# Performance work log

Hardware: AMD Instinct MI355X
Metric: run time of the kernel (lower is better)

Reference implementation:

```python
import jax, jax.numpy as jnp
import numpy as np

N_HEAD = 4
IN_FEAT = 512
N_FEAT = 512
D_K = N_FEAT // N_HEAD
KERNEL = 11
SANM_SHIFT = 0
LEFT_PAD = (KERNEL - 1) // 2 + SANM_SHIFT
RIGHT_PAD = KERNEL - 1 - LEFT_PAD
B, T = 16, 1024
NEG = -1e9  # stand-in for -inf (grad-safe)


def setup_inputs() -> dict:
    key = jax.random.key(0)
    ks = jax.random.split(key, 6)
    x = jax.random.normal(ks[0], (B, T, IN_FEAT), dtype=jnp.float32)
    # padding mask: first 3/4 of frames valid, tail padded (as in batched ASR)
    valid = (jnp.arange(T) < (3 * T) // 4).astype(jnp.float32)
    mask = jnp.broadcast_to(valid[None, None, :], (B, 1, T))
    s = 1.0 / np.sqrt(IN_FEAT)
    w_qkv = jax.random.uniform(ks[1], (IN_FEAT, 3 * N_FEAT), jnp.float32, -s, s)
    b_qkv = jnp.zeros((3 * N_FEAT,), jnp.float32)
    so = 1.0 / np.sqrt(N_FEAT)
    w_out = jax.random.uniform(ks[2], (N_FEAT, N_FEAT), jnp.float32, -so, so)
    b_out = jnp.zeros((N_FEAT,), jnp.float32)
    # depthwise Conv1d weight: (channels, k)
    w_fsmn = jax.random.uniform(ks[3], (N_FEAT, KERNEL), jnp.float32, -1.0 / np.sqrt(KERNEL), 1.0 / np.sqrt(KERNEL))
    return {"x": x, "mask": mask, "w_qkv": w_qkv, "b_qkv": b_qkv,
            "w_out": w_out, "b_out": b_out, "w_fsmn": w_fsmn}


def _fsmn(v, mask_bt1, w_fsmn):
    # v: (B,T,D); mask_bt1: (B,T,1)
    inp = v * mask_bt1
    xc = jnp.transpose(inp, (0, 2, 1))                      # (B,D,T)
    xc = jnp.pad(xc, ((0, 0), (0, 0), (LEFT_PAD, RIGHT_PAD)))
    y = jax.lax.conv_general_dilated(
        xc, w_fsmn[:, None, :], window_strides=(1,), padding='VALID',
        feature_group_count=N_FEAT, dimension_numbers=('NCH', 'OIH', 'NCH'))
    y = jnp.transpose(y, (0, 2, 1)) + inp                   # residual
    return y * mask_bt1                                     # re-zero padded frames


def _forward(x, mask, w_qkv, b_qkv, w_out, b_out, w_fsmn):
    b, t, _ = x.shape
    qkv = x @ w_qkv + b_qkv                                 # (B,T,3D)
    q, k, v = jnp.split(qkv, 3, axis=-1)
    qh = q.reshape(b, t, N_HEAD, D_K).transpose(0, 2, 1, 3) # (B,H,T,dk)
    kh = k.reshape(b, t, N_HEAD, D_K).transpose(0, 2, 1, 3)
    vh = v.reshape(b, t, N_HEAD, D_K).transpose(0, 2, 1, 3)

    fsmn_mem = _fsmn(v, mask.reshape(b, t, 1), w_fsmn)

    scale = D_K ** (-0.5)
    scores = jnp.einsum('bhqd,bhkd->bhqk', qh * scale, kh)  # (B,H,T,T)
    m0 = (mask[:, None, :, :] == 0)                         # (B,1,1,T)
    scores = jnp.where(m0, NEG, scores)
    attn = jax.nn.softmax(scores, axis=-1)
    attn = jnp.where(m0, 0.0, attn)
    ctx = jnp.einsum('bhqk,bhkd->bhqd', attn, vh)
    ctx = ctx.transpose(0, 2, 1, 3).reshape(b, t, N_FEAT)
    att_out = ctx @ w_out + b_out
    return att_out + fsmn_mem


def reference(x, mask, w_qkv, b_qkv, w_out, b_out, w_fsmn):
    return _forward(x, mask, w_qkv, b_qkv, w_out, b_out, w_fsmn)
```

## Files before the change

kernel.cpp:

```cpp
#include <hip/hip_runtime.h>
#include <stdint.h>

#define SCALE_Q 0.08838834764831845f
#define LOG2E 1.4426950408889634f
#define NEGBIG -1e30f

typedef __attribute__((ext_vector_type(4))) float f32x4;
typedef __attribute__((ext_vector_type(16))) float f32x16;
typedef __attribute__((ext_vector_type(8))) short s16x8;
typedef __attribute__((ext_vector_type(4))) unsigned u32x4;

static __device__ __forceinline__ unsigned short f2bf(float f) {
  unsigned int u = __builtin_bit_cast(unsigned int, f);
  u += 0x7FFFu + ((u >> 16) & 1u);
  return (unsigned short)(u >> 16);
}

static __device__ __forceinline__ unsigned cvt_pk_bf16(float lo, float hi) {
  unsigned r;
  asm("v_cvt_pk_bf16_f32 %0, %1, %2" : "=v"(r) : "v"(lo), "v"(hi));
  return r;
}

static __device__ __forceinline__ float xchg_max(float x) {
  float a = x, b = x;
  asm("v_permlane32_swap_b32 %0, %1" : "+v"(a), "+v"(b));
  return fmaxf(a, b);
}
static __device__ __forceinline__ float xchg_sum(float x) {
  float a = x, b = x;
  asm("v_permlane32_swap_b32 %0, %1" : "+v"(a), "+v"(b));
  return a + b;
}

static __device__ __forceinline__ float vmax16(const f32x16& v) {
  float a = fmaxf(fmaxf(fmaxf(v[0], v[1]), fmaxf(v[2], v[3])),
                  fmaxf(fmaxf(v[4], v[5]), fmaxf(v[6], v[7])));
  float b = fmaxf(fmaxf(fmaxf(v[8], v[9]), fmaxf(v[10], v[11])),
                  fmaxf(fmaxf(v[12], v[13]), fmaxf(v[14], v[15])));
  return fmaxf(a, b);
}

__global__ void k_convert_x(const float* __restrict__ x, unsigned short* __restrict__ xb) {
  int i = (blockIdx.x * 256 + threadIdx.x) * 8;
  const float4* p = reinterpret_cast<const float4*>(x + i);
  float4 a = p[0], b = p[1];
  s16x8 o;
  o[0] = f2bf(a.x); o[1] = f2bf(a.y); o[2] = f2bf(a.z); o[3] = f2bf(a.w);
  o[4] = f2bf(b.x); o[5] = f2bf(b.y); o[6] = f2bf(b.z); o[7] = f2bf(b.w);
  *reinterpret_cast<s16x8*>(xb + i) = o;
}

__global__ void k_transpose_bf(const float* __restrict__ w, unsigned short* __restrict__ wt, int Nd) {
  int gid = blockIdx.x * 256 + threadIdx.x;
  int n = gid >> 6;
  int k0 = (gid & 63) * 8;
  if (n >= Nd) return;
  s16x8 o;
#pragma unroll
  for (int j = 0; j < 8; ++j) o[j] = f2bf(w[(size_t)(k0 + j) * Nd + n]);
  *reinterpret_cast<s16x8*>(wt + (size_t)n * 512 + k0) = o;
}

template <int MODE>
__launch_bounds__(256, 2)
__global__ void k_gemm(const unsigned short* __restrict__ A,
                       const unsigned short* __restrict__ Bt,
                       const float* __restrict__ bias,
                       const float* __restrict__ fsmn,
                       unsigned short* __restrict__ qs, unsigned short* __restrict__ kbuf,
                       float* __restrict__ vf, unsigned short* __restrict__ vt,
                       float* __restrict__ outp,
                       int tiles_m) {
  __shared__ unsigned short a_lds[128 * 64];
  __shared__ unsigned short b_lds[128 * 64];
  int bid = blockIdx.x;
  int rb = bid % tiles_m, cb = bid / tiles_m;
  int tid = threadIdx.x;
  int w = tid >> 6, lane = tid & 63;
  int g = lane >> 4, ln = lane & 15;
  int wr = w >> 1, wc = w & 1;

  f32x4 acc[4][4] = {};

  for (int kb0 = 0; kb0 < 512; kb0 += 64) {
#pragma unroll
    for (int it = 0; it < 4; ++it) {
      int chunk = it * 256 + tid;
      int r = chunk >> 3, c = chunk & 7;
      s16x8 va = *reinterpret_cast<const s16x8*>(A + (size_t)(rb * 128 + r) * 512 + kb0 + c * 8);
      s16x8 vb = *reinterpret_cast<const s16x8*>(Bt + (size_t)(cb * 128 + r) * 512 + kb0 + c * 8);
      *reinterpret_cast<s16x8*>(a_lds + r * 64 + ((c ^ (r & 7)) * 8)) = va;
      *reinterpret_cast<s16x8*>(b_lds + r * 64 + ((c ^ (r & 7)) * 8)) = vb;
    }
    __syncthreads();
#pragma unroll
    for (int kk = 0; kk < 2; ++kk) {
      s16x8 af[4], bf[4];
#pragma unroll
      for (int m = 0; m < 4; ++m) {
        int row = wr * 64 + m * 16 + ln;
        af[m] = *reinterpret_cast<const s16x8*>(a_lds + row * 64 + ((kk * 32 + g * 8) ^ ((row & 7) * 8)));
      }
#pragma unroll
      for (int n = 0; n < 4; ++n) {
        int row = wc * 64 + n * 16 + ln;
        bf[n] = *reinterpret_cast<const s16x8*>(b_lds + row * 64 + ((kk * 32 + g * 8) ^ ((row & 7) * 8)));
      }
#pragma unroll
      for (int m = 0; m < 4; ++m)
#pragma unroll
        for (int n = 0; n < 4; ++n)
          acc[m][n] = __builtin_amdgcn_mfma_f32_16x16x32_bf16(af[m], bf[n], acc[m][n], 0, 0, 0);
    }
    __syncthreads();
  }

  int c0 = cb * 128;
  int R0 = rb * 128 + wr * 64;
#pragma unroll
  for (int m = 0; m < 4; ++m) {
#pragma unroll
    for (int n = 0; n < 4; ++n) {
      int col = c0 + wc * 64 + n * 16 + ln;
      int Rbase = R0 + m * 16 + g * 4;
      if constexpr (MODE == 0) {
        float bv = bias[col];
        int which = col >> 9;
        int h = (col >> 7) & 3;
        int d = col & 127;
        int b = Rbase >> 10, t0 = Rbase & 1023;
        if (which == 2) {
          unsigned short pk[4];
#pragma unroll
          for (int r = 0; r < 4; ++r) {
            float v = acc[m][n][r] + bv;
            vf[(size_t)(Rbase + r) * 512 + (col - 1024)] = v;
            pk[r] = f2bf(v);
          }
          uint2 uv;
          uv.x = (unsigned)pk[0] | ((unsigned)pk[1] << 16);
          uv.y = (unsigned)pk[2] | ((unsigned)pk[3] << 16);
          *reinterpret_cast<uint2*>(vt + ((size_t)((b * 4 + h) * 128 + d)) * 1024 + t0) = uv;
        } else {
          unsigned short* dst = (which == 0) ? qs : kbuf;
          float sc = (which == 0) ? (SCALE_Q * LOG2E) : 1.0f;
#pragma unroll
          for (int r = 0; r < 4; ++r) {
            int t = t0 + r;
            dst[((size_t)((b * 4 + h) * 1024 + t)) * 128 + d] = f2bf((acc[m][n][r] + bv) * sc);
          }
        }
      } else {
        float bv = bias[col];
#pragma unroll
        for (int r = 0; r < 4; ++r) {
          size_t idx = (size_t)(Rbase + r) * 512 + col;
          outp[idx] = acc[m][n][r] + bv + fsmn[idx];
        }
      }
    }
  }
}

__launch_bounds__(256, 2)
__global__ void k_fsmn(const float* __restrict__ vf, const float* __restrict__ mask,
                       const float* __restrict__ wf, float* __restrict__ out) {
  __shared__ float inp[266 * 64];
  __shared__ float wl[64 * 13];
  int bid = blockIdx.x;
  int b = bid >> 5;
  int tt = (bid >> 3) & 3;
  int dt = bid & 7;
  int t0 = tt * 256, d0 = dt * 64;
  int tid = threadIdx.x;
  if (tid < 64) {
#pragma unroll
    for (int j = 0; j < 11; ++j) wl[tid * 13 + j] = wf[(d0 + tid) * 11 + j];
  }
  for (int idx = tid; idx < 266 * 64; idx += 256) {
    int r = idx >> 6, c = idx & 63;
    int t = t0 - 5 + r;
    float v = 0.f;
    if (t >= 0 && t < 1024) v = vf[((size_t)b * 1024 + t) * 512 + d0 + c] * mask[b * 1024 + t];
    inp[idx] = v;
  }
  __syncthreads();
  for (int idx = tid; idx < 256 * 64; idx += 256) {
    int tr = idx >> 6, c = idx & 63;
    int t = t0 + tr;
    float acc = inp[(tr + 5) * 64 + c];
#pragma unroll
    for (int j = 0; j < 11; ++j) acc += inp[(tr + j) * 64 + c] * wl[c * 13 + j];
    out[((size_t)b * 1024 + t) * 512 + d0 + c] = acc * mask[b * 1024 + t];
  }
}

__launch_bounds__(512, 1)
__global__ void k_attn(const unsigned short* __restrict__ qs,
                       const unsigned short* __restrict__ kbuf,
                       const unsigned short* __restrict__ vt,
                       const float* __restrict__ mask,
                       unsigned short* __restrict__ ctx) {
  __shared__ unsigned short smem[2 * 128 * 128];
  __shared__ float mask_lds[128];
  unsigned short* k_lds = smem;
  unsigned short* vt_lds = smem + 128 * 128;

  int bid = blockIdx.x;
  int qc = bid & 3;
  int bh = bid >> 2;
  int b = bh >> 2, h = bh & 3;
  int tid = threadIdx.x;
  int w = tid >> 6, l = tid & 63;
  int half = l >> 5, lq = l & 31;

  const unsigned short* kbase = kbuf + (size_t)bh * 1024 * 128;
  const unsigned short* vtbase = vt + (size_t)bh * 128 * 1024;
  const float* mbase = mask + b * 1024;

  s16x8 aq[8];
  {
    const unsigned short* qrow = qs + ((size_t)bh * 1024 + qc * 256 + w * 32 + lq) * 128 + half * 8;
#pragma unroll
    for (int c = 0; c < 8; ++c)
      aq[c] = *reinterpret_cast<const s16x8*>(qrow + c * 16);
  }

  s16x8 bone = {};
  bone[0] = (short)(half == 0 ? 0x3F80 : 0);

  f32x16 o[4] = {};
  float M = NEGBIG, L = 0.f;

  for (int kb = 0; kb < 8; ++kb) {
    float m0 = mbase[kb * 128 + l];
    float m1 = mbase[kb * 128 + 64 + l];
    if (__ballot((m0 != 0.f) || (m1 != 0.f)) == 0ull) continue;

    __syncthreads();
#pragma unroll
    for (int it = 0; it < 4; ++it) {
      int chunk = it * 512 + tid;
      int r = chunk >> 4, c = chunk & 15;
      s16x8 kv = *reinterpret_cast<const s16x8*>(kbase + (size_t)(kb * 128 + r) * 128 + c * 8);
      *reinterpret_cast<s16x8*>(k_lds + r * 128 + ((c ^ (r & 15)) * 8)) = kv;
      s16x8 vv = *reinterpret_cast<const s16x8*>(vtbase + (size_t)r * 1024 + kb * 128 + c * 8);
      *reinterpret_cast<s16x8*>(vt_lds + r * 128 + ((c ^ (r & 15)) * 8)) = vv;
    }
    if (tid < 128) mask_lds[tid] = mbase[kb * 128 + tid];
    __syncthreads();

    f32x16 s[4];
#pragma unroll
    for (int kt = 0; kt < 4; ++kt) {
      float mv = mask_lds[kt * 32 + lq];
      s16x8 ba = {};
      ba[0] = (short)((half == 0 && mv == 0.f) ? (short)0xFF7F : 0);
      f32x16 z = {};
      s[kt] = __builtin_amdgcn_mfma_f32_32x32x16_bf16(ba, bone, z, 0, 0, 0);
      int row = kt * 32 + lq, rx = row & 15;
#pragma unroll
      for (int c = 0; c < 8; ++c) {
        s16x8 kf = *reinterpret_cast<const s16x8*>(k_lds + row * 128 + (((c * 2 + half) ^ rx) * 8));
        s[kt] = __builtin_amdgcn_mfma_f32_32x32x16_bf16(kf, aq[c], s[kt], 0, 0, 0);
      }
    }

    float mx = fmaxf(fmaxf(vmax16(s[0]), vmax16(s[1])), fmaxf(vmax16(s[2]), vmax16(s[3])));
    mx = xchg_max(mx);
    float mnew = fmaxf(M, mx);
    float alpha = exp2f(M - mnew);
    M = mnew;
    float ls0 = 0.f, ls1 = 0.f, ls2 = 0.f, ls3 = 0.f;
#pragma unroll
    for (int kt = 0; kt < 4; ++kt) {
#pragma unroll
      for (int i = 0; i < 16; ++i) {
        float p = exp2f(s[kt][i] - M);
        s[kt][i] = p;
        if ((i & 3) == 0) ls0 += p; else if ((i & 3) == 1) ls1 += p;
        else if ((i & 3) == 2) ls2 += p; else ls3 += p;
      }
    }
    float ls = (ls0 + ls1) + (ls2 + ls3);
    ls = xchg_sum(ls);
    L = L * alpha + ls;
#pragma unroll
    for (int dt = 0; dt < 4; ++dt)
#pragma unroll
      for (int i = 0; i < 16; ++i) o[dt][i] *= alpha;

#pragma unroll
    for (int kt = 0; kt < 4; ++kt) {
      unsigned w0 = cvt_pk_bf16(s[kt][0], s[kt][1]);
      unsigned w1 = cvt_pk_bf16(s[kt][2], s[kt][3]);
      unsigned w2 = cvt_pk_bf16(s[kt][4], s[kt][5]);
      unsigned w3 = cvt_pk_bf16(s[kt][6], s[kt][7]);
      unsigned w4 = cvt_pk_bf16(s[kt][8], s[kt][9]);
      unsigned w5 = cvt_pk_bf16(s[kt][10], s[kt][11]);
      unsigned w6 = cvt_pk_bf16(s[kt][12], s[kt][13]);
      unsigned w7 = cvt_pk_bf16(s[kt][14], s[kt][15]);
      asm("v_permlane32_swap_b32 %0, %1" : "+v"(w0), "+v"(w2));
      asm("v_permlane32_swap_b32 %0, %1" : "+v"(w1), "+v"(w3));
      asm("v_permlane32_swap_b32 %0, %1" : "+v"(w4), "+v"(w6));
      asm("v_permlane32_swap_b32 %0, %1" : "+v"(w5), "+v"(w7));
      u32x4 f0 = {w0, w1, w2, w3};
      u32x4 f1 = {w4, w5, w6, w7};
      s16x8 p0 = __builtin_bit_cast(s16x8, f0);
      s16x8 p1 = __builtin_bit_cast(s16x8, f1);
#pragma unroll
      for (int dt = 0; dt < 4; ++dt) {
        int row = dt * 32 + lq, rx = row & 15;
        s16x8 va = *reinterpret_cast<const s16x8*>(vt_lds + row * 128 + (((kt * 4 + half) ^ rx) * 8));
        o[dt] = __builtin_amdgcn_mfma_f32_32x32x16_bf16(va, p0, o[dt], 0, 0, 0);
        s16x8 vb = *reinterpret_cast<const s16x8*>(vt_lds + row * 128 + (((kt * 4 + 2 + half) ^ rx) * 8));
        o[dt] = __builtin_amdgcn_mfma_f32_32x32x16_bf16(vb, p1, o[dt], 0, 0, 0);
      }
    }
  }

  float inv = 1.0f / L;
  __syncthreads();
  unsigned short* obuf = smem;
#pragma unroll
  for (int dt = 0; dt < 4; ++dt) {
#pragma unroll
    for (int g = 0; g < 4; ++g) {
      int d0 = dt * 32 + g * 8 + half * 4;
      unsigned lo = cvt_pk_bf16(o[dt][g * 4 + 0] * inv, o[dt][g * 4 + 1] * inv);
      unsigned hi = cvt_pk_bf16(o[dt][g * 4 + 2] * inv, o[dt][g * 4 + 3] * inv);
      int row = w * 32 + lq;
      int gr = d0 >> 2;
      uint2 uv; uv.x = lo; uv.y = hi;
      *reinterpret_cast<uint2*>(obuf + row * 128 + ((gr ^ (row & 15)) * 4)) = uv;
    }
  }
  __syncthreads();
  size_t cbase = ((size_t)b * 1024 + qc * 256) * 512 + h * 128;
#pragma unroll
  for (int it = 0; it < 16; ++it) {
    int chunk = it * 512 + tid;
    int row = chunk >> 5, gr = chunk & 31;
    uint2 v = *reinterpret_cast<uint2*>(obuf + row * 128 + ((gr ^ (row & 15)) * 4));
    *reinterpret_cast<uint2*>(ctx + cbase + (size_t)row * 512 + gr * 4) = v;
  }
}

extern "C" void kernel_launch(void* const* d_in, const int* in_sizes, int n_in,
                              void* d_out, int out_size, void* d_ws, size_t ws_size,
                              hipStream_t stream) {
  const float* x      = (const float*)d_in[0];
  const float* mask   = (const float*)d_in[1];
  const float* w_qkv  = (const float*)d_in[2];
  const float* b_qkv  = (const float*)d_in[3];
  const float* w_out  = (const float*)d_in[4];
  const float* b_out  = (const float*)d_in[5];
  const float* w_fsmn = (const float*)d_in[6];
  float* out = (float*)d_out;

  char* ws = (char*)d_ws;
  size_t off = 0;
  auto alloc = [&](size_t bytes) { void* p = ws + off; off += (bytes + 255) & ~(size_t)255; return p; };
  unsigned short* x_bf   = (unsigned short*)alloc(16384ull * 512 * 2);
  unsigned short* wT_qkv = (unsigned short*)alloc(1536ull * 512 * 2);
  unsigned short* wT_out = (unsigned short*)alloc(512ull * 512 * 2);
  unsigned short* qs     = (unsigned short*)alloc(64ull * 1024 * 128 * 2);
  unsigned short* kbuf   = (unsigned short*)alloc(64ull * 1024 * 128 * 2);
  unsigned short* vt     = (unsigned short*)alloc(64ull * 128 * 1024 * 2);
  float*          vf     = (float*)alloc(16384ull * 512 * 4);
  float*          fsmn   = (float*)alloc(16384ull * 512 * 4);
  unsigned short* ctx    = (unsigned short*)alloc(16384ull * 512 * 2);

  k_convert_x<<<4096, 256, 0, stream>>>(x, x_bf);
  k_transpose_bf<<<(1536 * 64) / 256, 256, 0, stream>>>(w_qkv, wT_qkv, 1536);
  k_transpose_bf<<<(512 * 64) / 256, 256, 0, stream>>>(w_out, wT_out, 512);
  k_gemm<0><<<128 * 12, 256, 0, stream>>>(x_bf, wT_qkv, b_qkv, nullptr,
                                          qs, kbuf, vf, vt, nullptr, 128);
  k_fsmn<<<512, 256, 0, stream>>>(vf, mask, w_fsmn, fsmn);
  k_attn<<<256, 512, 0, stream>>>(qs, kbuf, vt, mask, ctx);
  k_gemm<1><<<128 * 4, 256, 0, stream>>>(ctx, wT_out, b_out, fsmn,
                                         nullptr, nullptr, nullptr, nullptr, out, 128);
}
```

Before: 245.5 us.

## Use direct global-to-LDS loads, double-buffer attention K/V, remap blocks, skip masked K/V tiles

The GEMM and attention staging now use global_load_lds so data is copied straight into shared memory without passing through registers. The attention kernel double-buffers K/V tiles over only the unmasked key blocks, so the next tile's load overlaps the current compute, and it raises wave priority around the MFMA sections. Block indices are remapped across the 8 XCDs in both kernels, and GEMM occupancy hints go up to 3 blocks per SM. The QKV GEMM also skips K/V column tiles whose rows are fully padded, which relies on those K/V rows never being read later, since the attention kernel skips masked keys and fsmn masks its input. That adds a dependency on the padding mask and leaves the skipped outputs uninitialised in the workspace.

Measured after the change: 267.0 us. +8.8%, slower.

```diff
diff --git a/kernel.cpp b/kernel.cpp
--- a/kernel.cpp
+++ b/kernel.cpp
@@ -39,6 +39,12 @@
   float b = fmaxf(fmaxf(fmaxf(v[8], v[9]), fmaxf(v[10], v[11])),
                   fmaxf(fmaxf(v[12], v[13]), fmaxf(v[14], v[15])));
   return fmaxf(a, b);
+}
+
+static __device__ __forceinline__ void gload16(const void* g, void* l) {
+  __builtin_amdgcn_global_load_lds(
+      (const __attribute__((address_space(1))) void*)g,
+      (__attribute__((address_space(3))) void*)l, 16, 0, 0);
 }
 
 __global__ void k_convert_x(const float* __restrict__ x, unsigned short* __restrict__ xb) {
@@ -63,35 +69,49 @@
 }
 
 template <int MODE>
-__launch_bounds__(256, 2)
+__launch_bounds__(256, 3)
 __global__ void k_gemm(const unsigned short* __restrict__ A,
                        const unsigned short* __restrict__ Bt,
                        const float* __restrict__ bias,
                        const float* __restrict__ fsmn,
+                       const float* __restrict__ mask,
                        unsigned short* __restrict__ qs, unsigned short* __restrict__ kbuf,
                        float* __restrict__ vf, unsigned short* __restrict__ vt,
                        float* __restrict__ outp,
-                       int tiles_m) {
+                       int tiles_m, int cpx) {
   __shared__ unsigned short a_lds[128 * 64];
   __shared__ unsigned short b_lds[128 * 64];
-  int bid = blockIdx.x;
+  int bid0 = blockIdx.x;
+  int bid = (bid0 & 7) * cpx + (bid0 >> 3);
   int rb = bid % tiles_m, cb = bid / tiles_m;
   int tid = threadIdx.x;
   int w = tid >> 6, lane = tid & 63;
   int g = lane >> 4, ln = lane & 15;
   int wr = w >> 1, wc = w & 1;
 
+  if constexpr (MODE == 0) {
+    if (cb >= 4) {
+      int b = (rb * 128) >> 10, t0 = (rb * 128) & 1023;
+      const float* mb = mask + b * 1024 + t0;
+      float a0 = mb[lane * 2], a1 = mb[lane * 2 + 1];
+      if (__ballot(a0 != 0.f || a1 != 0.f) == 0ull) return;
+    }
+  }
+
+  int sr = lane >> 3;
+  int sc = lane & 7;
+
   f32x4 acc[4][4] = {};
 
   for (int kb0 = 0; kb0 < 512; kb0 += 64) {
 #pragma unroll
     for (int it = 0; it < 4; ++it) {
-      int chunk = it * 256 + tid;
-      int r = chunk >> 3, c = chunk & 7;
-      s16x8 va = *reinterpret_cast<const s16x8*>(A + (size_t)(rb * 128 + r) * 512 + kb0 + c * 8);
-      s16x8 vb = *reinterpret_cast<const s16x8*>(Bt + (size_t)(cb * 128 + r) * 512 + kb0 + c * 8);
-      *reinterpret_cast<s16x8*>(a_lds + r * 64 + ((c ^ (r & 7)) * 8)) = va;
-      *reinterpret_cast<s16x8*>(b_lds + r * 64 + ((c ^ (r & 7)) * 8)) = vb;
+      int r = it * 32 + w * 8 + sr;
+      int cg = sc ^ (r & 7);
+      gload16(A + (size_t)(rb * 128 + r) * 512 + kb0 + cg * 8,
+              a_lds + (it * 32 + w * 8) * 64);
+      gload16(Bt + (size_t)(cb * 128 + r) * 512 + kb0 + cg * 8,
+              b_lds + (it * 32 + w * 8) * 64);
     }
     __syncthreads();
 #pragma unroll
@@ -100,12 +120,12 @@
 #pragma unroll
       for (int m = 0; m < 4; ++m) {
         int row = wr * 64 + m * 16 + ln;
-        af[m] = *reinterpret_cast<const s16x8*>(a_lds + row * 64 + ((kk * 32 + g * 8) ^ ((row & 7) * 8)));
+        af[m] = *reinterpret_cast<const s16x8*>(a_lds + row * 64 + (((kk * 4 + g) ^ (row & 7)) * 8));
       }
 #pragma unroll
       for (int n = 0; n < 4; ++n) {
         int row = wc * 64 + n * 16 + ln;
-        bf[n] = *reinterpret_cast<const s16x8*>(b_lds + row * 64 + ((kk * 32 + g * 8) ^ ((row & 7) * 8)));
+        bf[n] = *reinterpret_cast<const s16x8*>(b_lds + row * 64 + (((kk * 4 + g) ^ (row & 7)) * 8));
       }
 #pragma unroll
       for (int m = 0; m < 4; ++m)
@@ -144,11 +164,11 @@
           *reinterpret_cast<uint2*>(vt + ((size_t)((b * 4 + h) * 128 + d)) * 1024 + t0) = uv;
         } else {
           unsigned short* dst = (which == 0) ? qs : kbuf;
-          float sc = (which == 0) ? (SCALE_Q * LOG2E) : 1.0f;
+          float sc2 = (which == 0) ? (SCALE_Q * LOG2E) : 1.0f;
 #pragma unroll
           for (int r = 0; r < 4; ++r) {
             int t = t0 + r;
-            dst[((size_t)((b * 4 + h) * 1024 + t)) * 128 + d] = f2bf((acc[m][n][r] + bv) * sc);
+            dst[((size_t)((b * 4 + h) * 1024 + t)) * 128 + d] = f2bf((acc[m][n][r] + bv) * sc2);
           }
         }
       } else {
@@ -202,12 +222,10 @@
                        const unsigned short* __restrict__ vt,
                        const float* __restrict__ mask,
                        unsigned short* __restrict__ ctx) {
-  __shared__ unsigned short smem[2 * 128 * 128];
-  __shared__ float mask_lds[128];
-  unsigned short* k_lds = smem;
-  unsigned short* vt_lds = smem + 128 * 128;
-
-  int bid = blockIdx.x;
+  __shared__ unsigned short smem[2 * 32768];
+
+  int bid0 = blockIdx.x;
+  int bid = (bid0 & 7) * 32 + (bid0 >> 3);
   int qc = bid & 3;
   int bh = bid >> 2;
   int b = bh >> 2, h = bh & 3;
@@ -233,28 +251,46 @@
   f32x16 o[4] = {};
   float M = NEGBIG, L = 0.f;
 
+  unsigned amask = 0;
   for (int kb = 0; kb < 8; ++kb) {
     float m0 = mbase[kb * 128 + l];
     float m1 = mbase[kb * 128 + 64 + l];
-    if (__ballot((m0 != 0.f) || (m1 != 0.f)) == 0ull) continue;
-
-    __syncthreads();
+    if (__ballot((m0 != 0.f) || (m1 != 0.f)) != 0ull) amask |= (1u << kb);
+  }
+
+  auto stage = [&](int kb, int bsel) {
+    unsigned short* kd = smem + bsel * 32768;
+    unsigned short* vd = kd + 16384;
+    int srl = l >> 4;
+    int scl = l & 15;
 #pragma unroll
     for (int it = 0; it < 4; ++it) {
-      int chunk = it * 512 + tid;
-      int r = chunk >> 4, c = chunk & 15;
-      s16x8 kv = *reinterpret_cast<const s16x8*>(kbase + (size_t)(kb * 128 + r) * 128 + c * 8);
-      *reinterpret_cast<s16x8*>(k_lds + r * 128 + ((c ^ (r & 15)) * 8)) = kv;
-      s16x8 vv = *reinterpret_cast<const s16x8*>(vtbase + (size_t)r * 1024 + kb * 128 + c * 8);
-      *reinterpret_cast<s16x8*>(vt_lds + r * 128 + ((c ^ (r & 15)) * 8)) = vv;
-    }
-    if (tid < 128) mask_lds[tid] = mbase[kb * 128 + tid];
-    __syncthreads();
+      int r0 = it * 32 + w * 4;
+      int r = r0 + srl;
+      int cg = scl ^ (r & 15);
+      gload16(kbase + (size_t)(kb * 128 + r) * 128 + cg * 8, kd + r0 * 128);
+      gload16(vtbase + (size_t)r * 1024 + kb * 128 + cg * 8, vd + r0 * 128);
+    }
+  };
+
+  unsigned rem = amask;
+  int kb_cur = __ffs(rem) - 1; rem &= rem - 1;
+  stage(kb_cur, 0);
+  __syncthreads();
+  int cur = 0;
+
+  while (true) {
+    int kb_next = rem ? (__ffs(rem) - 1) : -1;
+    if (kb_next >= 0) { rem &= rem - 1; stage(kb_next, cur ^ 1); }
+
+    unsigned short* kl = smem + cur * 32768;
+    unsigned short* vl = kl + 16384;
 
     f32x16 s[4];
+    __builtin_amdgcn_s_setprio(1);
 #pragma unroll
     for (int kt = 0; kt < 4; ++kt) {
-      float mv = mask_lds[kt * 32 + lq];
+      float mv = mbase[kb_cur * 128 + kt * 32 + lq];
       s16x8 ba = {};
       ba[0] = (short)((half == 0 && mv == 0.f) ? (short)0xFF7F : 0);
       f32x16 z = {};
@@ -262,10 +298,11 @@
       int row = kt * 32 + lq, rx = row & 15;
 #pragma unroll
       for (int c = 0; c < 8; ++c) {
-        s16x8 kf = *reinterpret_cast<const s16x8*>(k_lds + row * 128 + (((c * 2 + half) ^ rx) * 8));
+        s16x8 kf = *reinterpret_cast<const s16x8*>(kl + row * 128 + (((c * 2 + half) ^ rx) * 8));
         s[kt] = __builtin_amdgcn_mfma_f32_32x32x16_bf16(kf, aq[c], s[kt], 0, 0, 0);
       }
     }
+    __builtin_amdgcn_s_setprio(0);
 
     float mx = fmaxf(fmaxf(vmax16(s[0]), vmax16(s[1])), fmaxf(vmax16(s[2]), vmax16(s[3])));
     mx = xchg_max(mx);
@@ -291,6 +328,7 @@
 #pragma unroll
       for (int i = 0; i < 16; ++i) o[dt][i] *= alpha;
 
+    __builtin_amdgcn_s_setprio(1);
 #pragma unroll
     for (int kt = 0; kt < 4; ++kt) {
       unsigned w0 = cvt_pk_bf16(s[kt][0], s[kt][1]);
@@ -312,12 +350,17 @@
 #pragma unroll
       for (int dt = 0; dt < 4; ++dt) {
         int row = dt * 32 + lq, rx = row & 15;
-        s16x8 va = *reinterpret_cast<const s16x8*>(vt_lds + row * 128 + (((kt * 4 + half) ^ rx) * 8));
+        s16x8 va = *reinterpret_cast<const s16x8*>(vl + row * 128 + (((kt * 4 + half) ^ rx) * 8));
         o[dt] = __builtin_amdgcn_mfma_f32_32x32x16_bf16(va, p0, o[dt], 0, 0, 0);
-        s16x8 vb = *reinterpret_cast<const s16x8*>(vt_lds + row * 128 + (((kt * 4 + 2 + half) ^ rx) * 8));
+        s16x8 vb = *reinterpret_cast<const s16x8*>(vl + row * 128 + (((kt * 4 + 2 + half) ^ rx) * 8));
         o[dt] = __builtin_amdgcn_mfma_f32_32x32x16_bf16(vb, p1, o[dt], 0, 0, 0);
       }
     }
+    __builtin_amdgcn_s_setprio(0);
+
+    if (kb_next < 0) break;
+    __syncthreads();
+    kb_cur = kb_next; cur ^= 1;
   }
 
   float inv = 1.0f / L;
@@ -375,10 +418,10 @@
   k_convert_x<<<4096, 256, 0, stream>>>(x, x_bf);
   k_transpose_bf<<<(1536 * 64) / 256, 256, 0, stream>>>(w_qkv, wT_qkv, 1536);
   k_transpose_bf<<<(512 * 64) / 256, 256, 0, stream>>>(w_out, wT_out, 512);
-  k_gemm<0><<<128 * 12, 256, 0, stream>>>(x_bf, wT_qkv, b_qkv, nullptr,
-                                          qs, kbuf, vf, vt, nullptr, 128);
+  k_gemm<0><<<128 * 12, 256, 0, stream>>>(x_bf, wT_qkv, b_qkv, nullptr, mask,
+                                          qs, kbuf, vf, vt, nullptr, 128, (128 * 12) / 8);
   k_fsmn<<<512, 256, 0, stream>>>(vf, mask, w_fsmn, fsmn);
   k_attn<<<256, 512, 0, stream>>>(qs, kbuf, vt, mask, ctx);
-  k_gemm<1><<<128 * 4, 256, 0, stream>>>(ctx, wT_out, b_out, fsmn,
-                                         nullptr, nullptr, nullptr, nullptr, out, 128);
-}
+  k_gemm<1><<<128 * 4, 256, 0, stream>>>(ctx, wT_out, b_out, fsmn, nullptr,
+                                         nullptr, nullptr, nullptr, nullptr, out, 128, (128 * 4) / 8);
+}
```
